# Kernel tuning notes

Hardware: AMD Instinct MI355X
Metric: run time of the kernel (lower is better)

The kernel has to match this reference:

```python
import jax, jax.numpy as jnp
import numpy as np

D_MODEL = 128
NEG_INF = -1e30


def setup_inputs() -> dict:
    key = jax.random.key(0)
    k1, k2, k3, k4 = jax.random.split(key, 4)
    B, Lc, Lq, d = 32, 2048, 256, D_MODEL
    C = jax.random.normal(k1, (B, Lc, d), dtype=jnp.float32)
    Q = jax.random.normal(k2, (B, Lq, d), dtype=jnp.float32)
    # Linear(3d, 1): weight laid out for cat order (Q_, C_, C_*Q_)
    w = jax.random.normal(k3, (3 * d,), dtype=jnp.float32) / np.sqrt(3 * d)
    b = jax.random.normal(k4, (1,), dtype=jnp.float32) * 0.01
    c_mask = jnp.ones((B, Lc), dtype=jnp.int32)
    q_mask = jnp.ones((B, Lq), dtype=jnp.int32)
    return {"C": C, "Q": Q, "w": w, "b": b, "c_mask": c_mask, "q_mask": q_mask}


def reference(C, Q, w, b, c_mask, q_mask):
    d = C.shape[-1]
    # Algebraic decomposition of Linear([Q_, C_, C_*Q_]) -> scalar:
    # S[b,i,j] = Q[b,j]@w_q + C[b,i]@w_c + (C[b,i]*w_m)@Q[b,j] + bias
    w_q, w_c, w_m = w[:d], w[d:2 * d], w[2 * d:]
    S = (C @ w_c)[:, :, None] \
        + (Q @ w_q)[:, None, :] \
        + jnp.einsum('bid,bjd->bij', C * w_m, Q) \
        + b[0]                                        # (B, Lc, Lq)
    mask = (c_mask[:, :, None] * q_mask[:, None, :]).astype(S.dtype)
    S = S * mask + NEG_INF * (1.0 - mask)
    S1 = jax.nn.softmax(S, axis=1)  # softmax over context dim (as in source)
    S2 = jax.nn.softmax(S, axis=2)  # softmax over query dim
    C2Q = jnp.einsum('bij,bjd->bid', S1, Q)           # (B, Lc, d)
    # Q2C = S1 @ S2^T @ C, associated as S1 @ (S2^T @ C) to avoid (Lc,Lc)
    T = jnp.einsum('bkj,bkd->bjd', S2, C)             # (B, Lq, d)
    Q2C = jnp.einsum('bij,bjd->bid', S1, T)           # (B, Lc, d)
    out = jnp.concatenate([C, C2Q, C * C2Q, C * Q2C], axis=2)  # (B, Lc, 4d)
    # dropout omitted (deterministic reference / eval mode)
    return out
```

## Files before the change

kernel.cpp:

```cpp
#include <hip/hip_runtime.h>


#define LC 2048
#define LQ 256
#define DM 128
#define NEG_INF_F (-1e30f)

using bf16x8  = __attribute__((ext_vector_type(8))) __bf16;
using f32x4   = __attribute__((ext_vector_type(4))) float;
using ushort8 = __attribute__((ext_vector_type(8))) unsigned short;

__device__ __forceinline__ unsigned short f2bf(float x) {
    unsigned int u = __float_as_uint(x);
    u += 0x7fffu + ((u >> 16) & 1u);
    return (unsigned short)(u >> 16);
}
__device__ __forceinline__ float bf2f(unsigned short h) {
    return __uint_as_float(((unsigned int)h) << 16);
}
__device__ __forceinline__ f32x4 mfma16(bf16x8 a, bf16x8 b, f32x4 c) {
    return __builtin_amdgcn_mfma_f32_16x16x32_bf16(a, b, c, 0, 0, 0);
}

__global__ __launch_bounds__(256) void k_preQ(const float* __restrict__ Q,
        const float* __restrict__ w, unsigned short* __restrict__ Qbf,
        unsigned short* __restrict__ Qt, float* __restrict__ rq) {
    const int b = blockIdx.z, j0 = blockIdx.x * 64, d0 = blockIdx.y * 64;
    const int tid = threadIdx.x;
    __shared__ float tile[64][65];
    __shared__ float wq[128];
    if (tid < 128) wq[tid] = w[tid];
    __syncthreads();
    const int r = tid >> 2, c0 = (tid & 3) * 16;
    const float4* sp = (const float4*)(Q + (size_t)(b * LQ + j0 + r) * DM + d0 + c0);
    float v[16];
#pragma unroll
    for (int u = 0; u < 4; ++u) {
        float4 t = sp[u];
        v[4*u] = t.x; v[4*u+1] = t.y; v[4*u+2] = t.z; v[4*u+3] = t.w;
    }
    unsigned short ob[16];
    float p = 0.f;
#pragma unroll
    for (int u = 0; u < 16; ++u) {
        ob[u] = f2bf(v[u]);
        p += v[u] * wq[d0 + c0 + u];
        tile[r][c0 + u] = v[u];
    }
    ushort8* qb = (ushort8*)(Qbf + (size_t)(b * LQ + j0 + r) * DM + d0 + c0);
    qb[0] = *(ushort8*)&ob[0];
    qb[1] = *(ushort8*)&ob[8];
    p += __shfl_xor(p, 1);
    p += __shfl_xor(p, 2);
    if ((tid & 3) == 0) atomicAdd(&rq[b * LQ + j0 + r], p);
    __syncthreads();
    unsigned short o[16];
#pragma unroll
    for (int u = 0; u < 16; ++u) o[u] = f2bf(tile[c0 + u][r]);
    ushort8* dp = (ushort8*)(Qt + (size_t)(b * DM + d0 + r) * LQ + j0 + c0);
    dp[0] = *(ushort8*)&o[0];
    dp[1] = *(ushort8*)&o[8];
}

__global__ __launch_bounds__(256) void k1_scores(
    const float* __restrict__ C, const unsigned short* __restrict__ Qbf,
    const float* __restrict__ w, const float* __restrict__ bptr,
    const int* __restrict__ c_mask, const int* __restrict__ q_mask,
    const float* __restrict__ rq,
    unsigned short* __restrict__ E, unsigned short* __restrict__ Ct,
    float* __restrict__ l1g, float* __restrict__ l2g) {
    const int b = blockIdx.y;
    const int i0 = blockIdx.x * 64;
    const int tid = threadIdx.x;
    const int lane = tid & 63, wid = tid >> 6;
    const int quad = lane >> 4, l15 = lane & 15;

    __shared__ unsigned short Alds[64][136];
    __shared__ float wsm[256];
    __shared__ float rcs[64], rqs[256], l2s[64];

    if (tid < 256) {
        wsm[tid] = w[128 + tid];
        const float qm = (float)q_mask[b * LQ + tid];
        rqs[tid] = (qm != 0.f) ? (rq[b * LQ + tid] + bptr[0]) : NEG_INF_F;
    }
    if (tid < 64) l2s[tid] = 0.f;
    __syncthreads();

    {
        const int r = tid >> 2, qq = tid & 3;
        const float4* cp = (const float4*)(C + (size_t)(b * LC + i0 + r) * DM + qq * 32);
        unsigned short* ctb = Ct + (size_t)b * DM * LC + i0 + r;
        float prc = 0.f;
#pragma unroll
        for (int u = 0; u < 8; ++u) {
            float4 v = cp[u];
            const int c0 = qq * 32 + u * 4;
            prc += v.x * wsm[c0] + v.y * wsm[c0 + 1] + v.z * wsm[c0 + 2] + v.w * wsm[c0 + 3];
            Alds[r][c0 + 0] = f2bf(v.x * wsm[128 + c0]);
            Alds[r][c0 + 1] = f2bf(v.y * wsm[129 + c0]);
            Alds[r][c0 + 2] = f2bf(v.z * wsm[130 + c0]);
            Alds[r][c0 + 3] = f2bf(v.w * wsm[131 + c0]);
            ctb[(size_t)(c0 + 0) * LC] = f2bf(v.x);
            ctb[(size_t)(c0 + 1) * LC] = f2bf(v.y);
            ctb[(size_t)(c0 + 2) * LC] = f2bf(v.z);
            ctb[(size_t)(c0 + 3) * LC] = f2bf(v.w);
        }
        prc += __shfl_xor(prc, 1);
        prc += __shfl_xor(prc, 2);
        if (qq == 0) {
            const float cmv = (float)c_mask[b * LC + i0 + r];
            rcs[r] = (cmv != 0.f) ? prc : NEG_INF_F;
        }
    }
    __syncthreads();

    const int n_base = wid * 64;
    const unsigned short* qbase = Qbf + (size_t)b * LQ * DM;
    const f32x4 z4 = {0.f, 0.f, 0.f, 0.f};
    f32x4 acc[4][4];
#pragma unroll
    for (int mt = 0; mt < 4; ++mt)
#pragma unroll
        for (int nt = 0; nt < 4; ++nt) acc[mt][nt] = z4;

#pragma unroll
    for (int kc = 0; kc < 4; ++kc) {
        const int ko = kc * 32 + quad * 8;
        bf16x8 af[4], bfr[4];
#pragma unroll
        for (int mt = 0; mt < 4; ++mt)
            af[mt] = *(const bf16x8*)&Alds[mt * 16 + l15][ko];
#pragma unroll
        for (int nt = 0; nt < 4; ++nt)
            bfr[nt] = *(const bf16x8*)(qbase + (size_t)(n_base + nt * 16 + l15) * DM + ko);
#pragma unroll
        for (int mt = 0; mt < 4; ++mt)
#pragma unroll
            for (int nt = 0; nt < 4; ++nt)
                acc[mt][nt] = mfma16(af[mt], bfr[nt], acc[mt][nt]);
    }

    float colsum[4] = {0.f, 0.f, 0.f, 0.f};
#pragma unroll
    for (int mt = 0; mt < 4; ++mt) {
#pragma unroll
        for (int reg = 0; reg < 4; ++reg) {
            const int m = mt * 16 + quad * 4 + reg;
            float rowsum = 0.f;
#pragma unroll
            for (int nt = 0; nt < 4; ++nt) {
                const int n = n_base + nt * 16 + l15;
                const float s = acc[mt][nt][reg] + rcs[m] + rqs[n];
                const float e = __expf(s);
                acc[mt][nt][reg] = e;
                rowsum += e;
                colsum[nt] += e;
            }
            rowsum += __shfl_xor(rowsum, 1);
            rowsum += __shfl_xor(rowsum, 2);
            rowsum += __shfl_xor(rowsum, 4);
            rowsum += __shfl_xor(rowsum, 8);
            if (l15 == 0) atomicAdd(&l2s[m], rowsum);
        }
    }
#pragma unroll
    for (int nt = 0; nt < 4; ++nt) {
        float v = colsum[nt];
        v += __shfl_xor(v, 16);
        v += __shfl_xor(v, 32);
        if (quad == 0) atomicAdd(&l1g[b * LQ + n_base + nt * 16 + l15], v);
    }
    __syncthreads();
    if (tid < 64) l2g[b * LC + i0 + tid] = l2s[tid];

#pragma unroll
    for (int mt = 0; mt < 4; ++mt) {
#pragma unroll
        for (int reg = 0; reg < 4; ++reg) {
            const int m = mt * 16 + quad * 4 + reg;
            const float rl = 1.0f / l2s[m];
            unsigned short* erow = E + (size_t)(b * LC + i0 + m) * LQ;
#pragma unroll
            for (int nt = 0; nt < 4; ++nt) {
                const int n = n_base + nt * 16 + l15;
                erow[n] = f2bf(acc[mt][nt][reg] * rl);
            }
        }
    }
}

__global__ __launch_bounds__(512) void k3_Tt(
    const unsigned short* __restrict__ E, const unsigned short* __restrict__ Ct,
    const unsigned short* __restrict__ Qt, const float* __restrict__ l1g,
    unsigned short* __restrict__ Qts, unsigned short* __restrict__ Tt) {
    const int id = blockIdx.x;
    const int t = id >> 3;
    const int jt = t & 3, dt = (t >> 2) & 1;
    const int b = ((t >> 3) << 3) | (id & 7);
    const int j0 = jt * 64, d0 = dt * 64;
    const int tid = threadIdx.x;
    const int lane = tid & 63, wid = tid >> 6;
    const int quad = lane >> 4, l15 = lane & 15;
    const int m_base = (wid >> 1) * 16, n32 = (wid & 1) * 32;

    __shared__ unsigned short Ab[64][136];
    __shared__ unsigned short Bb[64][136];
    __shared__ float rl1s[64];
    if (tid < 64) rl1s[tid] = 1.0f / l1g[b * LQ + j0 + tid];
    __syncthreads();

    if (dt == 0) {
        const int r = tid >> 2, jq = (tid & 3) * 16;
        const ushort8* qp = (const ushort8*)(Qt + (size_t)(b * DM + r) * LQ + j0 + jq);
        ushort8 v0 = qp[0], v1 = qp[1];
        unsigned short o[16];
#pragma unroll
        for (int u = 0; u < 8; ++u) o[u] = f2bf(bf2f(v0[u]) * rl1s[jq + u]);
#pragma unroll
        for (int u = 0; u < 8; ++u) o[8 + u] = f2bf(bf2f(v1[u]) * rl1s[jq + 8 + u]);
        ushort8* op = (ushort8*)(Qts + (size_t)(b * DM + r) * LQ + j0 + jq);
        op[0] = *(ushort8*)&o[0];
        op[1] = *(ushort8*)&o[8];
    }

    const f32x4 z4 = {0.f, 0.f, 0.f, 0.f};
    f32x4 acc[2] = {z4, z4};

    for (int it = 0; it < 16; ++it) {
        const int ic = it * 128;
        __syncthreads();
        {
            const int r = tid >> 3, q = tid & 7;
            const ushort8* cp = (const ushort8*)(Ct + (size_t)(b * DM + d0 + r) * LC + ic + q * 16);
            *(ushort8*)&Ab[r][q * 16] = cp[0];
            *(ushort8*)&Ab[r][q * 16 + 8] = cp[1];
        }
        {
            const int il = tid >> 2, sg = (tid & 3) * 16;
            const ushort8* ep = (const ushort8*)(E + (size_t)(b * LC + ic + il) * LQ + j0 + sg);
            ushort8 e0 = ep[0], e1 = ep[1];
#pragma unroll
            for (int u = 0; u < 8; ++u) Bb[sg + u][il] = e0[u];
#pragma unroll
            for (int u = 0; u < 8; ++u) Bb[sg + 8 + u][il] = e1[u];
        }
        __syncthreads();
#pragma unroll
        for (int kk = 0; kk < 4; ++kk) {
            const int ko = kk * 32 + quad * 8;
            bf16x8 af = *(const bf16x8*)&Ab[m_base + l15][ko];
            bf16x8 b0f = *(const bf16x8*)&Bb[n32 + l15][ko];
            bf16x8 b1f = *(const bf16x8*)&Bb[n32 + 16 + l15][ko];
            acc[0] = mfma16(af, b0f, acc[0]);
            acc[1] = mfma16(af, b1f, acc[1]);
        }
    }
#pragma unroll
    for (int nt = 0; nt < 2; ++nt)
#pragma unroll
        for (int reg = 0; reg < 4; ++reg) {
            const int dd = d0 + m_base + quad * 4 + reg;
            const int jl = n32 + nt * 16 + l15;
            Tt[(size_t)(b * DM + dd) * LQ + j0 + jl] = f2bf(acc[nt][reg] * rl1s[jl]);
        }
}

__global__ __launch_bounds__(256) void k4_out(
    const unsigned short* __restrict__ E, const float* __restrict__ C,
    const unsigned short* __restrict__ Qts, const unsigned short* __restrict__ Tt,
    const float* __restrict__ l2g, float* __restrict__ out) {
    const int id = blockIdx.x;
    const int b = (id & 7) | ((id >> 8) << 3);
    const int i0 = ((id >> 3) & 31) * 64;
    const int tid = threadIdx.x;
    const int lane = tid & 63, wid = tid >> 6;
    const int quad = lane >> 4, l15 = lane & 15;
    const int n_base = wid * 32;

    __shared__ unsigned short Aq[64][264];
    __shared__ float l2s[64];
    if (tid < 64) l2s[tid] = l2g[b * LC + i0 + tid];

    {
        const int r = tid >> 2, c0 = (tid & 3) * 64;
        const ushort8* ep = (const ushort8*)(E + (size_t)(b * LC + i0 + r) * LQ + c0);
#pragma unroll
        for (int u = 0; u < 8; ++u) *(ushort8*)&Aq[r][c0 + u * 8] = ep[u];
    }
    __syncthreads();

    const unsigned short* qsb = Qts + (size_t)b * DM * LQ;
    const unsigned short* ttb = Tt  + (size_t)b * DM * LQ;
    const f32x4 z4 = {0.f, 0.f, 0.f, 0.f};
    f32x4 acc1[4][2], acc2[4][2];
#pragma unroll
    for (int mt = 0; mt < 4; ++mt)
#pragma unroll
        for (int nt = 0; nt < 2; ++nt) { acc1[mt][nt] = z4; acc2[mt][nt] = z4; }

#pragma unroll 2
    for (int ks = 0; ks < 8; ++ks) {
        const int ko = ks * 32 + quad * 8;
        bf16x8 a[4], bq[2], bt[2];
#pragma unroll
        for (int mt = 0; mt < 4; ++mt)
            a[mt] = *(const bf16x8*)&Aq[mt * 16 + l15][ko];
#pragma unroll
        for (int nt = 0; nt < 2; ++nt) {
            const size_t roff = (size_t)(n_base + nt * 16 + l15) * LQ + ko;
            bq[nt] = *(const bf16x8*)(qsb + roff);
            bt[nt] = *(const bf16x8*)(ttb + roff);
        }
#pragma unroll
        for (int mt = 0; mt < 4; ++mt)
#pragma unroll
            for (int nt = 0; nt < 2; ++nt) {
                acc1[mt][nt] = mfma16(a[mt], bq[nt], acc1[mt][nt]);
                acc2[mt][nt] = mfma16(a[mt], bt[nt], acc2[mt][nt]);
            }
    }

#pragma unroll
    for (int mt = 0; mt < 4; ++mt)
#pragma unroll
        for (int reg = 0; reg < 4; ++reg) {
            const int il = mt * 16 + quad * 4 + reg;
            const int i = i0 + il;
            const float l2v = l2s[il];
            const size_t rb = (size_t)(b * LC + i) * 512;
            const float* crow = C + (size_t)(b * LC + i) * DM;
#pragma unroll
            for (int nt = 0; nt < 2; ++nt) {
                const int d = n_base + nt * 16 + l15;
                const float c = crow[d];
                const float v1 = acc1[mt][nt][reg] * l2v;
                const float v2 = acc2[mt][nt][reg] * l2v;
                out[rb + d] = c;
                out[rb + 128 + d] = v1;
                out[rb + 256 + d] = c * v1;
                out[rb + 384 + d] = c * v2;
            }
        }
}

extern "C" void kernel_launch(void* const* d_in, const int* in_sizes, int n_in,
                              void* d_out, int out_size, void* d_ws, size_t ws_size,
                              hipStream_t stream) {
    const float* C = (const float*)d_in[0];
    const float* Q = (const float*)d_in[1];
    const float* w = (const float*)d_in[2];
    const float* bp = (const float*)d_in[3];
    const int* cm = (const int*)d_in[4];
    const int* qm = (const int*)d_in[5];
    float* out = (float*)d_out;

    char* ws = (char*)d_ws;
    unsigned short* E   = (unsigned short*)(ws);
    unsigned short* Ct  = (unsigned short*)(ws + 33554432);
    unsigned short* Qbf = (unsigned short*)(ws + 50331648);
    unsigned short* Qt  = (unsigned short*)(ws + 52428800);
    unsigned short* Qts = (unsigned short*)(ws + 54525952);
    unsigned short* Tt  = (unsigned short*)(ws + 56623104);
    float*          l2g = (float*)(ws + 58720256);
    float*          rq  = (float*)(ws + 58982400);
    float*          l1  = (float*)(ws + 59015168);

    hipMemsetAsync(ws + 58982400, 0, 65536, stream);

    k_preQ<<<dim3(4, 2, 32), 256, 0, stream>>>(Q, w, Qbf, Qt, rq);
    k1_scores<<<dim3(32, 32), 256, 0, stream>>>(C, Qbf, w, bp, cm, qm, rq, E, Ct, l1, l2g);
    k3_Tt<<<dim3(256), 512, 0, stream>>>(E, Ct, Qt, l1, Qts, Tt);
    k4_out<<<dim3(1024), 256, 0, stream>>>(E, C, Qts, Tt, l2g, out);
}
```

Baseline: 241.8 us.

## Write transposed score matrix in k1 and read MFMA operands directly from global in k3

The score kernel now also writes a transposed bf16 copy of the normalized scores (Et, laid out j-major over context). k3 then loads its MFMA A and B fragments straight from global memory (Ct and Et rows) instead of staging tiles through LDS with a scalar transposing scatter, which removes the shared-memory buffers and per-iteration barriers. The cost is an extra 32 MB of 8-byte strided writes in k1, plus k3 loads that rely on cache rather than LDS reuse. The 16-byte loads in k3 are strided across rows, so coalescing may suffer.

Measured after the change: 278.8 us. 15.3% more time.

```diff
diff --git a/kernel.cpp b/kernel.cpp
--- a/kernel.cpp
+++ b/kernel.cpp
@@ -6,9 +6,10 @@
 #define DM 128
 #define NEG_INF_F (-1e30f)
 
-using bf16x8  = __attribute__((ext_vector_type(8))) __bf16;
-using f32x4   = __attribute__((ext_vector_type(4))) float;
-using ushort8 = __attribute__((ext_vector_type(8))) unsigned short;
+using bf16x8   = __attribute__((ext_vector_type(8))) __bf16;
+using f32x4    = __attribute__((ext_vector_type(4))) float;
+using ushort8  = __attribute__((ext_vector_type(8))) unsigned short;
+using ushort4v = __attribute__((ext_vector_type(4))) unsigned short;
 
 __device__ __forceinline__ unsigned short f2bf(float x) {
     unsigned int u = __float_as_uint(x);
@@ -67,7 +68,8 @@
     const float* __restrict__ w, const float* __restrict__ bptr,
     const int* __restrict__ c_mask, const int* __restrict__ q_mask,
     const float* __restrict__ rq,
-    unsigned short* __restrict__ E, unsigned short* __restrict__ Ct,
+    unsigned short* __restrict__ E, unsigned short* __restrict__ Et,
+    unsigned short* __restrict__ Ct,
     float* __restrict__ l1g, float* __restrict__ l2g) {
     const int b = blockIdx.y;
     const int i0 = blockIdx.x * 64;
@@ -176,22 +178,35 @@
 
 #pragma unroll
     for (int mt = 0; mt < 4; ++mt) {
+        float rl4[4];
+#pragma unroll
+        for (int reg = 0; reg < 4; ++reg)
+            rl4[reg] = 1.0f / l2s[mt * 16 + quad * 4 + reg];
 #pragma unroll
         for (int reg = 0; reg < 4; ++reg) {
             const int m = mt * 16 + quad * 4 + reg;
-            const float rl = 1.0f / l2s[m];
             unsigned short* erow = E + (size_t)(b * LC + i0 + m) * LQ;
 #pragma unroll
             for (int nt = 0; nt < 4; ++nt) {
                 const int n = n_base + nt * 16 + l15;
-                erow[n] = f2bf(acc[mt][nt][reg] * rl);
+                erow[n] = f2bf(acc[mt][nt][reg] * rl4[reg]);
             }
         }
+#pragma unroll
+        for (int nt = 0; nt < 4; ++nt) {
+            const int j = n_base + nt * 16 + l15;
+            unsigned short o4[4];
+#pragma unroll
+            for (int reg = 0; reg < 4; ++reg)
+                o4[reg] = f2bf(acc[mt][nt][reg] * rl4[reg]);
+            *(ushort4v*)(Et + (size_t)(b * LQ + j) * LC + i0 + mt * 16 + quad * 4)
+                = *(ushort4v*)o4;
+        }
     }
 }
 
 __global__ __launch_bounds__(512) void k3_Tt(
-    const unsigned short* __restrict__ E, const unsigned short* __restrict__ Ct,
+    const unsigned short* __restrict__ Et, const unsigned short* __restrict__ Ct,
     const unsigned short* __restrict__ Qt, const float* __restrict__ l1g,
     unsigned short* __restrict__ Qts, unsigned short* __restrict__ Tt) {
     const int id = blockIdx.x;
@@ -204,8 +219,6 @@
     const int quad = lane >> 4, l15 = lane & 15;
     const int m_base = (wid >> 1) * 16, n32 = (wid & 1) * 32;
 
-    __shared__ unsigned short Ab[64][136];
-    __shared__ unsigned short Bb[64][136];
     __shared__ float rl1s[64];
     if (tid < 64) rl1s[tid] = 1.0f / l1g[b * LQ + j0 + tid];
     __syncthreads();
@@ -224,38 +237,23 @@
         op[1] = *(ushort8*)&o[8];
     }
 
+    const unsigned short* arow  = Ct + (size_t)(b * DM + d0 + m_base + l15) * LC + quad * 8;
+    const unsigned short* brow0 = Et + (size_t)(b * LQ + j0 + n32 + l15) * LC + quad * 8;
+    const unsigned short* brow1 = Et + (size_t)(b * LQ + j0 + n32 + 16 + l15) * LC + quad * 8;
+
     const f32x4 z4 = {0.f, 0.f, 0.f, 0.f};
     f32x4 acc[2] = {z4, z4};
 
-    for (int it = 0; it < 16; ++it) {
-        const int ic = it * 128;
-        __syncthreads();
-        {
-            const int r = tid >> 3, q = tid & 7;
-            const ushort8* cp = (const ushort8*)(Ct + (size_t)(b * DM + d0 + r) * LC + ic + q * 16);
-            *(ushort8*)&Ab[r][q * 16] = cp[0];
-            *(ushort8*)&Ab[r][q * 16 + 8] = cp[1];
-        }
-        {
-            const int il = tid >> 2, sg = (tid & 3) * 16;
-            const ushort8* ep = (const ushort8*)(E + (size_t)(b * LC + ic + il) * LQ + j0 + sg);
-            ushort8 e0 = ep[0], e1 = ep[1];
-#pragma unroll
-            for (int u = 0; u < 8; ++u) Bb[sg + u][il] = e0[u];
-#pragma unroll
-            for (int u = 0; u < 8; ++u) Bb[sg + 8 + u][il] = e1[u];
-        }
-        __syncthreads();
-#pragma unroll
-        for (int kk = 0; kk < 4; ++kk) {
-            const int ko = kk * 32 + quad * 8;
-            bf16x8 af = *(const bf16x8*)&Ab[m_base + l15][ko];
-            bf16x8 b0f = *(const bf16x8*)&Bb[n32 + l15][ko];
-            bf16x8 b1f = *(const bf16x8*)&Bb[n32 + 16 + l15][ko];
-            acc[0] = mfma16(af, b0f, acc[0]);
-            acc[1] = mfma16(af, b1f, acc[1]);
-        }
-    }
+#pragma unroll 4
+    for (int kc = 0; kc < 64; ++kc) {
+        const int ko = kc * 32;
+        bf16x8 af  = *(const bf16x8*)(arow + ko);
+        bf16x8 b0f = *(const bf16x8*)(brow0 + ko);
+        bf16x8 b1f = *(const bf16x8*)(brow1 + ko);
+        acc[0] = mfma16(af, b0f, acc[0]);
+        acc[1] = mfma16(af, b1f, acc[1]);
+    }
+
 #pragma unroll
     for (int nt = 0; nt < 2; ++nt)
 #pragma unroll
@@ -365,11 +363,12 @@
     float*          l2g = (float*)(ws + 58720256);
     float*          rq  = (float*)(ws + 58982400);
     float*          l1  = (float*)(ws + 59015168);
+    unsigned short* Et  = (unsigned short*)(ws + 59047936);
 
     hipMemsetAsync(ws + 58982400, 0, 65536, stream);
 
     k_preQ<<<dim3(4, 2, 32), 256, 0, stream>>>(Q, w, Qbf, Qt, rq);
-    k1_scores<<<dim3(32, 32), 256, 0, stream>>>(C, Qbf, w, bp, cm, qm, rq, E, Ct, l1, l2g);
-    k3_Tt<<<dim3(256), 512, 0, stream>>>(E, Ct, Qt, l1, Qts, Tt);
+    k1_scores<<<dim3(32, 32), 256, 0, stream>>>(C, Qbf, w, bp, cm, qm, rq, E, Et, Ct, l1, l2g);
+    k3_Tt<<<dim3(256), 512, 0, stream>>>(Et, Ct, Qt, l1, Qts, Tt);
     k4_out<<<dim3(1024), 256, 0, stream>>>(E, C, Qts, Tt, l2g, out);
 }
```

## Retile Tt kernel to more smaller blocks and fold Q scaling into output kernel

Applied to the files above, without the earlier changes.

The T^T kernel now launches twice as many 256-thread blocks, each covering 32 query columns instead of 64, to improve CU coverage. The per-column 1/l1 scaling of Q is no longer written out as a separate Qts buffer; the output kernel instead scales Qt on the fly while loading its MFMA operand. This removes one intermediate write and read, but it adds conversion ALU work in k4's inner loop and doubles the context-tile loads in k3.

New measurement: 240.2 us. Within noise of the previous version (-0.7%).

```diff
diff --git a/kernel.cpp b/kernel.cpp
--- a/kernel.cpp
+++ b/kernel.cpp
@@ -6,9 +6,9 @@
 #define DM 128
 #define NEG_INF_F (-1e30f)
 
-using bf16x8  = __attribute__((ext_vector_type(8))) __bf16;
-using f32x4   = __attribute__((ext_vector_type(4))) float;
-using ushort8 = __attribute__((ext_vector_type(8))) unsigned short;
+using bf16x8   = __attribute__((ext_vector_type(8))) __bf16;
+using f32x4    = __attribute__((ext_vector_type(4))) float;
+using ushort8  = __attribute__((ext_vector_type(8))) unsigned short;
 
 __device__ __forceinline__ unsigned short f2bf(float x) {
     unsigned int u = __float_as_uint(x);
@@ -190,39 +190,24 @@
     }
 }
 
-__global__ __launch_bounds__(512) void k3_Tt(
+__global__ __launch_bounds__(256) void k3_Tt(
     const unsigned short* __restrict__ E, const unsigned short* __restrict__ Ct,
-    const unsigned short* __restrict__ Qt, const float* __restrict__ l1g,
-    unsigned short* __restrict__ Qts, unsigned short* __restrict__ Tt) {
+    const float* __restrict__ l1g, unsigned short* __restrict__ Tt) {
     const int id = blockIdx.x;
-    const int t = id >> 3;
-    const int jt = t & 3, dt = (t >> 2) & 1;
-    const int b = ((t >> 3) << 3) | (id & 7);
-    const int j0 = jt * 64, d0 = dt * 64;
+    const int rest = id >> 3;
+    const int jt = rest & 7;
+    const int dt = (rest >> 3) & 1;
+    const int b  = ((rest >> 4) << 3) | (id & 7);
+    const int j0 = jt * 32, d0 = dt * 64;
     const int tid = threadIdx.x;
     const int lane = tid & 63, wid = tid >> 6;
     const int quad = lane >> 4, l15 = lane & 15;
-    const int m_base = (wid >> 1) * 16, n32 = (wid & 1) * 32;
+    const int m_base = wid * 16;
 
     __shared__ unsigned short Ab[64][136];
-    __shared__ unsigned short Bb[64][136];
-    __shared__ float rl1s[64];
-    if (tid < 64) rl1s[tid] = 1.0f / l1g[b * LQ + j0 + tid];
-    __syncthreads();
-
-    if (dt == 0) {
-        const int r = tid >> 2, jq = (tid & 3) * 16;
-        const ushort8* qp = (const ushort8*)(Qt + (size_t)(b * DM + r) * LQ + j0 + jq);
-        ushort8 v0 = qp[0], v1 = qp[1];
-        unsigned short o[16];
-#pragma unroll
-        for (int u = 0; u < 8; ++u) o[u] = f2bf(bf2f(v0[u]) * rl1s[jq + u]);
-#pragma unroll
-        for (int u = 0; u < 8; ++u) o[8 + u] = f2bf(bf2f(v1[u]) * rl1s[jq + 8 + u]);
-        ushort8* op = (ushort8*)(Qts + (size_t)(b * DM + r) * LQ + j0 + jq);
-        op[0] = *(ushort8*)&o[0];
-        op[1] = *(ushort8*)&o[8];
-    }
+    __shared__ unsigned short Bb[32][136];
+    __shared__ float rl1s[32];
+    if (tid < 32) rl1s[tid] = 1.0f / l1g[b * LQ + j0 + tid];
 
     const f32x4 z4 = {0.f, 0.f, 0.f, 0.f};
     f32x4 acc[2] = {z4, z4};
@@ -231,13 +216,15 @@
         const int ic = it * 128;
         __syncthreads();
         {
-            const int r = tid >> 3, q = tid & 7;
-            const ushort8* cp = (const ushort8*)(Ct + (size_t)(b * DM + d0 + r) * LC + ic + q * 16);
-            *(ushort8*)&Ab[r][q * 16] = cp[0];
-            *(ushort8*)&Ab[r][q * 16 + 8] = cp[1];
+            const int r = tid >> 2, q = (tid & 3) * 32;
+            const ushort8* cp = (const ushort8*)(Ct + (size_t)(b * DM + d0 + r) * LC + ic + q);
+            *(ushort8*)&Ab[r][q]      = cp[0];
+            *(ushort8*)&Ab[r][q + 8]  = cp[1];
+            *(ushort8*)&Ab[r][q + 16] = cp[2];
+            *(ushort8*)&Ab[r][q + 24] = cp[3];
         }
         {
-            const int il = tid >> 2, sg = (tid & 3) * 16;
+            const int il = tid >> 1, sg = (tid & 1) * 16;
             const ushort8* ep = (const ushort8*)(E + (size_t)(b * LC + ic + il) * LQ + j0 + sg);
             ushort8 e0 = ep[0], e1 = ep[1];
 #pragma unroll
@@ -249,9 +236,9 @@
 #pragma unroll
         for (int kk = 0; kk < 4; ++kk) {
             const int ko = kk * 32 + quad * 8;
-            bf16x8 af = *(const bf16x8*)&Ab[m_base + l15][ko];
-            bf16x8 b0f = *(const bf16x8*)&Bb[n32 + l15][ko];
-            bf16x8 b1f = *(const bf16x8*)&Bb[n32 + 16 + l15][ko];
+            bf16x8 af  = *(const bf16x8*)&Ab[m_base + l15][ko];
+            bf16x8 b0f = *(const bf16x8*)&Bb[l15][ko];
+            bf16x8 b1f = *(const bf16x8*)&Bb[16 + l15][ko];
             acc[0] = mfma16(af, b0f, acc[0]);
             acc[1] = mfma16(af, b1f, acc[1]);
         }
@@ -261,15 +248,16 @@
 #pragma unroll
         for (int reg = 0; reg < 4; ++reg) {
             const int dd = d0 + m_base + quad * 4 + reg;
-            const int jl = n32 + nt * 16 + l15;
+            const int jl = nt * 16 + l15;
             Tt[(size_t)(b * DM + dd) * LQ + j0 + jl] = f2bf(acc[nt][reg] * rl1s[jl]);
         }
 }
 
 __global__ __launch_bounds__(256) void k4_out(
     const unsigned short* __restrict__ E, const float* __restrict__ C,
-    const unsigned short* __restrict__ Qts, const unsigned short* __restrict__ Tt,
-    const float* __restrict__ l2g, float* __restrict__ out) {
+    const unsigned short* __restrict__ Qt, const unsigned short* __restrict__ Tt,
+    const float* __restrict__ l1g, const float* __restrict__ l2g,
+    float* __restrict__ out) {
     const int id = blockIdx.x;
     const int b = (id & 7) | ((id >> 8) << 3);
     const int i0 = ((id >> 3) & 31) * 64;
@@ -280,7 +268,9 @@
 
     __shared__ unsigned short Aq[64][264];
     __shared__ float l2s[64];
+    __shared__ float rl1s[256];
     if (tid < 64) l2s[tid] = l2g[b * LC + i0 + tid];
+    rl1s[tid] = 1.0f / l1g[b * LQ + tid];
 
     {
         const int r = tid >> 2, c0 = (tid & 3) * 64;
@@ -290,8 +280,8 @@
     }
     __syncthreads();
 
-    const unsigned short* qsb = Qts + (size_t)b * DM * LQ;
-    const unsigned short* ttb = Tt  + (size_t)b * DM * LQ;
+    const unsigned short* qtb = Qt + (size_t)b * DM * LQ;
+    const unsigned short* ttb = Tt + (size_t)b * DM * LQ;
     const f32x4 z4 = {0.f, 0.f, 0.f, 0.f};
     f32x4 acc1[4][2], acc2[4][2];
 #pragma unroll
@@ -309,7 +299,12 @@
 #pragma unroll
         for (int nt = 0; nt < 2; ++nt) {
             const size_t roff = (size_t)(n_base + nt * 16 + l15) * LQ + ko;
-            bq[nt] = *(const bf16x8*)(qsb + roff);
+            const ushort8 qr = *(const ushort8*)(qtb + roff);
+            unsigned short qs[8];
+#pragma unroll
+            for (int e = 0; e < 8; ++e)
+                qs[e] = f2bf(bf2f(qr[e]) * rl1s[ko + e]);
+            bq[nt] = *(const bf16x8*)qs;
             bt[nt] = *(const bf16x8*)(ttb + roff);
         }
 #pragma unroll
@@ -360,7 +355,6 @@
     unsigned short* Ct  = (unsigned short*)(ws + 33554432);
     unsigned short* Qbf = (unsigned short*)(ws + 50331648);
     unsigned short* Qt  = (unsigned short*)(ws + 52428800);
-    unsigned short* Qts = (unsigned short*)(ws + 54525952);
     unsigned short* Tt  = (unsigned short*)(ws + 56623104);
     float*          l2g = (float*)(ws + 58720256);
     float*          rq  = (float*)(ws + 58982400);
@@ -370,6 +364,6 @@
 
     k_preQ<<<dim3(4, 2, 32), 256, 0, stream>>>(Q, w, Qbf, Qt, rq);
     k1_scores<<<dim3(32, 32), 256, 0, stream>>>(C, Qbf, w, bp, cm, qm, rq, E, Ct, l1, l2g);
-    k3_Tt<<<dim3(256), 512, 0, stream>>>(E, Ct, Qt, l1, Qts, Tt);
-    k4_out<<<dim3(1024), 256, 0, stream>>>(E, C, Qts, Tt, l2g, out);
-}
+    k3_Tt<<<dim3(512), 256, 0, stream>>>(E, Ct, l1, Tt);
+    k4_out<<<dim3(1024), 256, 0, stream>>>(E, C, Qt, Tt, l1, l2g, out);
+}
```
